# Optimization experiments

Measured on AMD Instinct MI355X. Metric: run time of the kernel, lower is better.

Reference implementation:

```python
import jax, jax.numpy as jnp
import numpy as np

B, T, X, H, Z, Y, G = 4096, 32, 256, 256, 128, 2, 128


def setup_inputs() -> dict:
    key = jax.random.key(0)
    ks = jax.random.split(key, 16)
    rn = lambda k, s, sc=0.05: jax.random.normal(k, s, dtype=jnp.float32) * sc
    n_days = jnp.concatenate([jnp.array([T], dtype=jnp.int32),
                              jax.random.randint(ks[2], (B - 1,), 1, T + 1).astype(jnp.int32)])
    return {
        "x": rn(ks[0], (B, T, X), 1.0),
        "y_true": jax.nn.softmax(jax.random.normal(ks[1], (B, T, Y), dtype=jnp.float32), axis=-1),
        "n_days": n_days,
        "z0": rn(ks[3], (B, Z), 1.0),
        "eps": rn(ks[4], (T, B, Z), 1.0),
        "W_ih": rn(ks[5], (3 * H, X)), "W_hh": rn(ks[6], (3 * H, H)),
        "b_ih": jnp.zeros((3 * H,), jnp.float32), "b_hh": jnp.zeros((3 * H,), jnp.float32),
        "Wph": rn(ks[7], (Z, X + H + Z)), "bph": jnp.zeros((Z,), jnp.float32),
        "Woh": rn(ks[8], (Z, X + H + Y + Z)), "boh": jnp.zeros((Z,), jnp.float32),
        "Wpm": rn(ks[9], (Z, Z)), "bpm": jnp.zeros((Z,), jnp.float32),
        "Wps": rn(ks[10], (Z, Z)), "bps": jnp.zeros((Z,), jnp.float32),
        "Wqm": rn(ks[11], (Z, Z)), "bqm": jnp.zeros((Z,), jnp.float32),
        "Wqs": rn(ks[12], (Z, Z)), "bqs": jnp.zeros((Z,), jnp.float32),
        "Wg": rn(ks[13], (G, H + Z)), "bg": jnp.zeros((G,), jnp.float32),
        "Wy": rn(ks[14], (Y, G)), "by": jnp.zeros((Y,), jnp.float32),
    }


def _forward(x, y_true, z0, eps, W_ih, W_hh, b_ih, b_hh, Wph, bph, Woh, boh,
             Wpm, bpm, Wps, bps, Wqm, bqm, Wqs, bqs, Wg, bg, Wy, by, n_days):
    xt = jnp.transpose(x, (1, 0, 2))       # [T, B, X]
    yt = jnp.transpose(y_true, (1, 0, 2))  # [T, B, Y]

    # --- GRU over time (torch nn.GRU gate math) ---
    def gru_step(h, xi):
        gi = xi @ W_ih.T + b_ih
        gh = h @ W_hh.T + b_hh
        ir, iz, inn = jnp.split(gi, 3, axis=-1)
        hr, hz, hn = jnp.split(gh, 3, axis=-1)
        r = jax.nn.sigmoid(ir + hr)
        u = jax.nn.sigmoid(iz + hz)
        n = jnp.tanh(inn + r * hn)
        h_new = (1.0 - u) * n + u * h
        return h_new, h_new

    h0 = jnp.zeros((x.shape[0], H), x.dtype)
    _, hs = jax.lax.scan(gru_step, h0, xt)  # [T, B, H]
    # pack/pad semantics: padded timesteps produce zero outputs
    valid = jnp.arange(T)[:, None] < n_days[None, :]  # [T, B]
    hs = jnp.where(valid[:, :, None], hs, 0.0)

    # --- sequential VAE latent scan: z_t depends on z_{t-1} ---
    def vmd_step(z, inputs):
        xi, hi, yi, ei = inputs
        hzp = jnp.tanh(jnp.concatenate([xi, hi, z], -1) @ Wph.T + bph)
        mp = hzp @ Wpm.T + bpm
        sp = jnp.sqrt(jnp.exp(hzp @ Wps.T + bps))
        hzq = jnp.tanh(jnp.concatenate([xi, hi, yi, z], -1) @ Woh.T + boh)
        mq = hzq @ Wqm.T + bqm
        sq = jnp.sqrt(jnp.exp(hzq @ Wqs.T + bqs))
        z_post = mq + sq * ei
        # kl_normal_normal(post || prior)
        kl = jnp.log(sp / sq) + (sq * sq + (mq - mp) ** 2) / (2.0 * sp * sp) - 0.5
        return z_post, (z_post, kl)

    _, (z_posts, kls_e) = jax.lax.scan(vmd_step, z0, (xt, hs, yt, eps))
    kls = jnp.sum(kls_e, axis=-1).T  # [B, T]

    hz = jnp.concatenate([jnp.transpose(hs, (1, 0, 2)),
                          jnp.transpose(z_posts, (1, 0, 2))], -1)  # [B, T, H+Z]
    g = jnp.tanh(hz @ Wg.T + bg)                     # [B, T, G]
    y_pred = jax.nn.softmax(g @ Wy.T + by, axis=-1)  # [B, T, Y]

    idx = n_days - 1
    b = jnp.arange(x.shape[0])
    g_T = g[b, idx]       # [B, G]
    y_T = y_pred[b, idx]  # [B, Y]
    return jnp.concatenate([g_T, y_T, kls], axis=-1)  # [B, G+Y+T]


def reference(x, y_true, n_days, z0, eps, W_ih, W_hh, b_ih, b_hh, Wph, bph,
              Woh, boh, Wpm, bpm, Wps, bps, Wqm, bqm, Wqs, bqs, Wg, bg, Wy, by):
    return _forward(x, y_true, z0, eps, W_ih, W_hh, b_ih, b_hh, Wph, bph, Woh,
                    boh, Wpm, bpm, Wps, bps, Wqm, bqm, Wqs, bqs, Wg, bg, Wy, by,
                    n_days)
```

## Files before the change

kernel.cpp:

```cpp
#include <hip/hip_runtime.h>

typedef unsigned short u16;
typedef short bf16x8 __attribute__((ext_vector_type(8)));
typedef float f32x4 __attribute__((ext_vector_type(4)));

__device__ __forceinline__ float bf2f(u16 v){
  union { unsigned u; float f; } x; x.u = ((unsigned)v) << 16; return x.f;
}
__device__ __forceinline__ u16 f2bf(float f){
  union { float f; unsigned u; } x; x.f = f;
  unsigned u = x.u;
  u += 0x7fffu + ((u >> 16) & 1u);
  return (u16)(u >> 16);
}
__device__ __forceinline__ unsigned pk_bf16(float lo, float hi){
  unsigned r;
  asm volatile("v_cvt_pk_bf16_f32 %0, %1, %2" : "=v"(r) : "v"(lo), "v"(hi));
  return r;
}
__device__ __forceinline__ float sigm(float x){ return 1.f/(1.f+__expf(-x)); }
__device__ __forceinline__ float tanh_s(float x){ return 1.f - 2.f/(__expf(2.f*x)+1.f); }
__device__ __forceinline__ f32x4 mfma16(bf16x8 a, bf16x8 b, f32x4 c){
  return __builtin_amdgcn_mfma_f32_16x16x32_bf16(a, b, c, 0, 0, 0);
}
__device__ __forceinline__ void gl2lds16(const void* g, void* l){
  __builtin_amdgcn_global_load_lds(
      (const __attribute__((address_space(1))) unsigned int*)g,
      (__attribute__((address_space(3))) unsigned int*)l, 16, 0, 0);
}

__global__ void prep_w(const float* __restrict__ W_ih, const float* __restrict__ W_hh,
                       const float* __restrict__ Wph, const float* __restrict__ Woh,
                       const float* __restrict__ Wpm, const float* __restrict__ Wps,
                       const float* __restrict__ Wqm, const float* __restrict__ Wqs,
                       const float* __restrict__ Wg,  const float* __restrict__ bph,
                       const float* __restrict__ boh,
                       u16* __restrict__ wsb, float* __restrict__ Woy, float* __restrict__ bpq)
{
  int idx = blockIdx.x*256 + threadIdx.x;
  if (idx < 196608){ wsb[idx] = f2bf(W_ih[idx]); return; }
  if (idx < 393216){ wsb[idx] = f2bf(W_hh[idx-196608]); return; }
  if (idx < 524288){ int j = idx-393216; int row = j>>9, col = j&511;
    float v = (row<128) ? Wph[row*640+col] : Woh[(row-128)*642+col];
    wsb[idx] = f2bf(v); return; }
  if (idx < 540672){ int j = idx-524288; int row=j>>7, col=j&127; wsb[idx]=f2bf(Wph[row*640+512+col]); return; }
  if (idx < 557056){ int j = idx-540672; int row=j>>7, col=j&127; wsb[idx]=f2bf(Woh[row*642+514+col]); return; }
  if (idx < 573440){ wsb[idx]=f2bf(Wpm[idx-557056]); return; }
  if (idx < 589824){ wsb[idx]=f2bf(Wps[idx-573440]); return; }
  if (idx < 606208){ wsb[idx]=f2bf(Wqm[idx-589824]); return; }
  if (idx < 622592){ wsb[idx]=f2bf(Wqs[idx-606208]); return; }
  if (idx < 671744){ wsb[idx]=f2bf(Wg[idx-622592]); return; }
  if (idx < 672000){ int j = idx-671744; int row=j>>1; Woy[j] = Woh[row*642+512+(j&1)]; return; }
  if (idx < 672256){ int j = idx-672000; bpq[j] = (j<128) ? bph[j] : boh[j-128]; return; }
}

__global__ void prep_b(const float* __restrict__ b_ih, const float* __restrict__ b_hh,
                       float* __restrict__ bsum)
{
  int j = threadIdx.x;
  if (j < 768) bsum[j] = b_ih[j] + (j < 512 ? b_hh[j] : 0.f);
}

__global__ void prep_x(const float* __restrict__ x, u16* __restrict__ xbf){
  int i = blockIdx.x*256 + threadIdx.x;
  if (i >= 4194304) return;
  const float4* src = (const float4*)(x + (size_t)i*8);
  float4 a = src[0], b = src[1];
  uint4 o;
  o.x = pk_bf16(a.x, a.y);
  o.y = pk_bf16(a.z, a.w);
  o.z = pk_bf16(b.x, b.y);
  o.w = pk_bf16(b.z, b.w);
  ((uint4*)xbf)[i] = o;
}

__global__ __launch_bounds__(512, 4) void gemm_bt(
  const u16* __restrict__ A1, const u16* __restrict__ A2, int K1, int Ktot,
  const u16* __restrict__ W, const float* __restrict__ bias,
  u16* __restrict__ C, int N, int mode,
  const float* __restrict__ yt, const float* __restrict__ Woy)
{
  const int m0 = blockIdx.x*128;
  const int n0 = blockIdx.y*256;
  const int tid = threadIdx.x;
  const int w = tid>>6, lane = tid&63, c = lane&15, g = lane>>4;
  const int wm = w>>2, wn = w&3;
  const int K2 = Ktot - K1;
  __shared__ __align__(16) u16 abuf[8*128*8];
  __shared__ __align__(16) u16 wbuf[8*256*8];
  f32x4 acc[4][4];
  #pragma unroll
  for (int i=0;i<4;++i)
    #pragma unroll
    for (int j=0;j<4;++j) acc[i][j] = (f32x4){0.f,0.f,0.f,0.f};
  const int nch = Ktot >> 6;
  for (int kc=0; kc<nch; ++kc){
    __syncthreads();
    #pragma unroll
    for (int i=0;i<2;++i){
      int ii = w*2 + i;
      int p = ii*64 + lane;
      int k8 = p>>7, row = p&127;
      int k = (kc<<6) + k8*8;
      const u16* src = (k < K1) ? (A1 + (size_t)(m0+row)*K1 + k)
                                : (A2 + (size_t)(m0+row)*K2 + (k-K1));
      gl2lds16(src, &abuf[ii*512]);
    }
    #pragma unroll
    for (int i=0;i<4;++i){
      int ii = w*4 + i;
      int p = ii*64 + lane;
      int k8 = p>>8, row = p&255;
      int k = (kc<<6) + k8*8;
      const u16* src = W + (size_t)(n0+row)*Ktot + k;
      gl2lds16(src, &wbuf[ii*512]);
    }
    __syncthreads();
    #pragma unroll
    for (int ks=0;ks<2;++ks){
      int k8 = ks*4 + g;
      bf16x8 a[4];
      #pragma unroll
      for (int mt=0;mt<4;++mt) a[mt] = *(const bf16x8*)&abuf[(k8*128 + wm*64 + mt*16 + c)*8];
      #pragma unroll
      for (int nt=0;nt<4;++nt){
        bf16x8 b = *(const bf16x8*)&wbuf[(k8*256 + wn*64 + nt*16 + c)*8];
        #pragma unroll
        for (int mt=0;mt<4;++mt)
          acc[mt][nt] = mfma16(a[mt], b, acc[mt][nt]);
      }
    }
  }
  #pragma unroll
  for (int nt=0;nt<4;++nt){
    int n = n0 + wn*64 + nt*16 + c;
    float bn = bias[n];
    float wy0 = 0.f, wy1 = 0.f;
    bool yfl = (mode==1) && (n >= 128);
    if (yfl){ wy0 = Woy[(n-128)*2]; wy1 = Woy[(n-128)*2+1]; }
    #pragma unroll
    for (int mt=0;mt<4;++mt){
      #pragma unroll
      for (int r=0;r<4;++r){
        size_t m = (size_t)m0 + wm*64 + mt*16 + g*4 + r;
        float v = acc[mt][nt][r] + bn;
        if (yfl) v += yt[2*m]*wy0 + yt[2*m+1]*wy1;
        C[m*(size_t)N + n] = f2bf(v);
      }
    }
  }
}

__global__ __launch_bounds__(1024) void gru_seq(
  const u16* __restrict__ GI, const u16* __restrict__ Whh,
  const float* __restrict__ bhh, const int* __restrict__ n_days,
  u16* __restrict__ hs)
{
  const int b0 = blockIdx.x*16;
  const int tid = threadIdx.x;
  const int w = tid>>6, lane = tid&63, c = lane&15, g = lane>>4;
  const int j0 = w*16 + g*4;
  __shared__ __align__(16) u16 hbuf[2][32*16*8];
  __shared__ __align__(16) u16 gibuf[3][16*768];
  __shared__ float bhnl[256];

  bf16x8 wa[3][8];
  #pragma unroll
  for (int gate=0; gate<3; ++gate)
    #pragma unroll
    for (int ks=0; ks<8; ++ks)
      wa[gate][ks] = *(const bf16x8*)&Whh[(size_t)(gate*256 + w*16 + c)*256 + ks*32 + g*8];

  if (tid < 256) bhnl[tid] = bhh[512 + tid];
  const int ndc = n_days[b0 + c];

  int so0, so1;
  { int pe = w*512 + lane*8; int row = pe/768, off = pe%768;
    so0 = (b0+row)*32*768 + (off ^ ((row&7)<<3)); }
  { int pe = (16+w)*512 + lane*8; int row = pe/768, off = pe%768;
    so1 = (b0+row)*32*768 + (off ^ ((row&7)<<3)); }
  const int rd0 = c*1536 + ((j0*2) ^ ((c&7)<<4));
  const int hroff = (g*16 + c)*16;
  const int hwoff = ((w*2 + (g>>1))*16 + c)*16 + (g&1)*8;
  u16* hsp = hs + ((size_t)(b0+c)*32)*256 + j0;

  float hprev[4] = {0.f,0.f,0.f,0.f};
  if (tid < 512) ((uint4*)hbuf[0])[tid] = make_uint4(0,0,0,0);

  gl2lds16(GI + so0,       (char*)gibuf[0] + w*1024);
  if (w < 8) gl2lds16(GI + so1, (char*)gibuf[0] + (16+w)*1024);
  gl2lds16(GI + so0 + 768, (char*)gibuf[1] + w*1024);
  if (w < 8) gl2lds16(GI + so1 + 768, (char*)gibuf[1] + (16+w)*1024);
  asm volatile("s_waitcnt vmcnt(0)" ::: "memory");
  __syncthreads();

  const u16* hr = hbuf[0];
  u16*       hw = hbuf[1];
  int cur = 0;
  #pragma unroll 1
  for (int t=0; t<32; ++t){
    if (t < 30){
      int nxt3 = cur >= 1 ? cur-1 : 2;
      const u16* gp = GI + (t+2)*768;
      gl2lds16(gp + so0, (char*)gibuf[nxt3] + w*1024);
      if (w < 8) gl2lds16(gp + so1, (char*)gibuf[nxt3] + (16+w)*1024);
    }
    if (t < 30){
      if (w < 8) asm volatile("s_waitcnt vmcnt(3)" ::: "memory");
      else       asm volatile("s_waitcnt vmcnt(2)" ::: "memory");
    } else if (t == 30){
      asm volatile("s_waitcnt vmcnt(1)" ::: "memory");
    }
    __builtin_amdgcn_sched_barrier(0);
    f32x4 aR = (f32x4){0.f,0.f,0.f,0.f};
    f32x4 aU = (f32x4){0.f,0.f,0.f,0.f};
    float4 bhn4 = *(const float4*)&bhnl[j0];
    f32x4 aN = (f32x4){bhn4.x, bhn4.y, bhn4.z, bhn4.w};
    #pragma unroll
    for (int ks=0; ks<8; ++ks){
      bf16x8 hf = *(const bf16x8*)((const char*)hr + hroff + ks*1024);
      aR = mfma16(wa[0][ks], hf, aR);
      aU = mfma16(wa[1][ks], hf, aU);
      aN = mfma16(wa[2][ks], hf, aN);
    }
    {
      const char* gib = (const char*)gibuf[cur];
      ushort4 gr_ = *(const ushort4*)(gib + rd0);
      ushort4 gu_ = *(const ushort4*)(gib + rd0 + 512);
      ushort4 gn_ = *(const ushort4*)(gib + rd0 + 1024);
      float h4[4];
      #pragma unroll
      for (int r=0; r<4; ++r){
        u16 grv = r==0?gr_.x : r==1?gr_.y : r==2?gr_.z : gr_.w;
        u16 guv = r==0?gu_.x : r==1?gu_.y : r==2?gu_.z : gu_.w;
        u16 gnv = r==0?gn_.x : r==1?gn_.y : r==2?gn_.z : gn_.w;
        float rr = sigm(bf2f(grv) + aR[r]);
        float uu = sigm(bf2f(guv) + aU[r]);
        float nn = tanh_s(bf2f(gnv) + rr*aN[r]);
        float h = nn + uu*(hprev[r]-nn);
        hprev[r] = h;
        h4[r] = h;
      }
      uint2 hpk;
      hpk.x = pk_bf16(h4[0], h4[1]);
      hpk.y = pk_bf16(h4[2], h4[3]);
      *(uint2*)((char*)hw + hwoff) = hpk;
      uint2 hst = (t < ndc) ? hpk : make_uint2(0u,0u);
      *(uint2*)(hsp + t*256) = hst;
    }
    asm volatile("s_waitcnt lgkmcnt(0)" ::: "memory");
    __builtin_amdgcn_sched_barrier(0);
    __builtin_amdgcn_s_barrier();
    __builtin_amdgcn_sched_barrier(0);
    { const u16* tmp = hr; hr = hw; hw = (u16*)tmp; }
    cur = cur==2 ? 0 : cur+1;
  }
}

__global__ __launch_bounds__(512) void vae_seq(
  const u16* __restrict__ HPQ, const float* __restrict__ z0,
  const float* __restrict__ eps, const int* __restrict__ n_days,
  const u16* __restrict__ Wm,
  const float* __restrict__ bpm, const float* __restrict__ bps,
  const float* __restrict__ bqm, const float* __restrict__ bqs,
  u16* __restrict__ zidx, float* __restrict__ out)
{
  const int b0 = blockIdx.x*16;
  const int tid = threadIdx.x, w = tid>>6, lane = tid&63, c = lane&15, g = lane>>4;
  const int j0 = w*16 + g*4;
  __shared__ __align__(16) u16 zbuf[16*16*8];
  __shared__ __align__(16) u16 hzpb[16*16*8];
  __shared__ __align__(16) u16 hzqb[16*16*8];
  __shared__ __align__(16) char hpql[3][8192];
  __shared__ __align__(16) char epsl[3][8192];
  __shared__ float klb[32][16][8];

  bf16x8 wf[6][4];
  #pragma unroll
  for (int mat=0;mat<6;++mat)
    #pragma unroll
    for (int ks=0;ks<4;++ks)
      wf[mat][ks] = *(const bf16x8*)&Wm[mat*16384 + (w*16+c)*128 + ks*32 + g*8];

  const float4 bpm4 = *(const float4*)(bpm + j0);
  const float4 bps4 = *(const float4*)(bps + j0);
  const float4 bqm4 = *(const float4*)(bqm + j0);
  const float4 bqs4 = *(const float4*)(bqs + j0);
  const int ndc = n_days[b0 + c];

  int soH, soE;
  { int p = (w*64 + lane)*16; int row = p/512, off = p%512;
    int so = off ^ ((row&7)<<4);
    soH = (b0+row)*32*256 + (so>>1);
    soE = (b0+row)*128 + (so>>2); }
  const int rdH = c*512 + ((j0*2) ^ ((c&7)<<4));
  const int rdE = c*512 + ((j0*4) ^ ((c&7)<<4));
  const int hroff = (g*16 + c)*16;
  const int hwoff = ((w*2 + (g>>1))*16 + c)*16 + (g&1)*8;

  if (tid < 256){
    int k8 = tid>>4, row = tid&15;
    const float* zp = z0 + (size_t)(b0+row)*128 + k8*8;
    uint4 o;
    o.x = pk_bf16(zp[0], zp[1]);
    o.y = pk_bf16(zp[2], zp[3]);
    o.z = pk_bf16(zp[4], zp[5]);
    o.w = pk_bf16(zp[6], zp[7]);
    ((uint4*)zbuf)[tid] = o;
  }
  gl2lds16(HPQ + soH,        hpql[0] + w*1024);
  gl2lds16(eps + soE,        epsl[0] + w*1024);
  gl2lds16(HPQ + soH + 256,  hpql[1] + w*1024);
  gl2lds16(eps + soE + 524288, epsl[1] + w*1024);
  asm volatile("s_waitcnt vmcnt(0)" ::: "memory");
  __syncthreads();

  uint2 zsel = make_uint2(0u,0u);
  int cur = 0;
  #pragma unroll 1
  for (int t=0; t<32; ++t){
    if (t < 30){
      int nxt3 = cur >= 1 ? cur-1 : 2;
      gl2lds16(HPQ + soH + (t+2)*256,           hpql[nxt3] + w*1024);
      gl2lds16(eps + soE + (size_t)(t+2)*524288, epsl[nxt3] + w*1024);
    }
    if (t < 30)      { asm volatile("s_waitcnt vmcnt(2)" ::: "memory"); }
    else if (t == 30){ asm volatile("s_waitcnt vmcnt(0)" ::: "memory"); }
    __builtin_amdgcn_sched_barrier(0);
    f32x4 accP = (f32x4){0,0,0,0}, accQ = (f32x4){0,0,0,0};
    #pragma unroll
    for (int ks=0;ks<4;++ks){
      bf16x8 zf = *(const bf16x8*)((const char*)zbuf + hroff + ks*1024);
      accP = mfma16(wf[0][ks], zf, accP);
      accQ = mfma16(wf[1][ks], zf, accQ);
    }
    {
      const char* hb_ = hpql[cur];
      ushort4 hp4 = *(const ushort4*)(hb_ + rdH);
      ushort4 hq4 = *(const ushort4*)(hb_ + rdH + 256);
      float p4[4], q4[4];
      #pragma unroll
      for (int r=0;r<4;++r){
        u16 pv = r==0?hp4.x : r==1?hp4.y : r==2?hp4.z : hp4.w;
        u16 qv = r==0?hq4.x : r==1?hq4.y : r==2?hq4.z : hq4.w;
        p4[r] = tanh_s(bf2f(pv) + accP[r]);
        q4[r] = tanh_s(bf2f(qv) + accQ[r]);
      }
      uint2 ppk, qpk;
      ppk.x = pk_bf16(p4[0], p4[1]);  ppk.y = pk_bf16(p4[2], p4[3]);
      qpk.x = pk_bf16(q4[0], q4[1]);  qpk.y = pk_bf16(q4[2], q4[3]);
      *(uint2*)((char*)hzpb + hwoff) = ppk;
      *(uint2*)((char*)hzqb + hwoff) = qpk;
    }
    asm volatile("s_waitcnt lgkmcnt(0)" ::: "memory");
    __builtin_amdgcn_sched_barrier(0);
    __builtin_amdgcn_s_barrier();
    __builtin_amdgcn_sched_barrier(0);
    {
      f32x4 aMP=(f32x4){0,0,0,0}, aAP=(f32x4){0,0,0,0};
      f32x4 aMQ=(f32x4){0,0,0,0}, aAQ=(f32x4){0,0,0,0};
      #pragma unroll
      for (int ks=0;ks<4;++ks){
        bf16x8 pf = *(const bf16x8*)((const char*)hzpb + hroff + ks*1024);
        bf16x8 qf = *(const bf16x8*)((const char*)hzqb + hroff + ks*1024);
        aMP = mfma16(wf[2][ks], pf, aMP);
        aAP = mfma16(wf[3][ks], pf, aAP);
        aMQ = mfma16(wf[4][ks], qf, aMQ);
        aAQ = mfma16(wf[5][ks], qf, aAQ);
      }
      float4 e4 = *(const float4*)(epsl[cur] + rdE);
      float kls = 0.f;
      float z4[4];
      #pragma unroll
      for (int r=0;r<4;++r){
        float mp = aMP[r]+(r==0?bpm4.x:r==1?bpm4.y:r==2?bpm4.z:bpm4.w);
        float ap = aAP[r]+(r==0?bps4.x:r==1?bps4.y:r==2?bps4.z:bps4.w);
        float mq = aMQ[r]+(r==0?bqm4.x:r==1?bqm4.y:r==2?bqm4.z:bqm4.w);
        float aq = aAQ[r]+(r==0?bqs4.x:r==1?bqs4.y:r==2?bqs4.z:bqs4.w);
        float ev = r==0?e4.x : r==1?e4.y : r==2?e4.z : e4.w;
        float z = mq + __expf(0.5f*aq)*ev;
        float d = mq - mp;
        kls += 0.5f*(ap-aq) + 0.5f*(__expf(aq)+d*d)*__expf(-ap) - 0.5f;
        z4[r] = z;
      }
      uint2 zpk;
      zpk.x = pk_bf16(z4[0], z4[1]);
      zpk.y = pk_bf16(z4[2], z4[3]);
      *(uint2*)((char*)zbuf + hwoff) = zpk;
      if (t == ndc-1) zsel = zpk;
      kls += __shfl_xor(kls, 16);
      kls += __shfl_xor(kls, 32);
      if (lane < 16) klb[t][c][w] = kls;
    }
    asm volatile("s_waitcnt lgkmcnt(0)" ::: "memory");
    __builtin_amdgcn_sched_barrier(0);
    __builtin_amdgcn_s_barrier();
    __builtin_amdgcn_sched_barrier(0);
    cur = cur==2 ? 0 : cur+1;
  }
  *(uint2*)(zidx + (size_t)(b0+c)*128 + j0) = zsel;
  {
    int t2 = tid>>4, c2 = tid&15;
    float s = 0.f;
    #pragma unroll
    for (int ww=0;ww<8;++ww) s += klb[t2][c2][ww];
    out[(size_t)(b0+c2)*162 + 130 + t2] = s;
  }
}

__global__ __launch_bounds__(128) void head_k(
  const u16* __restrict__ hs, const u16* __restrict__ zidx,
  const int* __restrict__ n_days, const u16* __restrict__ Wgb,
  const float* __restrict__ bg, const float* __restrict__ Wy,
  const float* __restrict__ by, float* __restrict__ out)
{
  const int b = blockIdx.x;
  const int tid = threadIdx.x;
  const int lane = tid & 63, wv = tid >> 6;
  __shared__ float hz[384];
  __shared__ float red[2][2];
  const int idx = n_days[b]-1;
  const u16* hrow = hs + ((size_t)b*32 + idx)*256;
  for (int k=tid; k<256; k+=128) hz[k] = bf2f(hrow[k]);
  hz[256+tid] = bf2f(zidx[(size_t)b*128 + tid]);
  __syncthreads();
  const u16* wrow = Wgb + (size_t)tid*384;
  float s = 0.f;
  #pragma unroll 4
  for (int k8=0;k8<48;++k8){
    bf16x8 wvv = *(const bf16x8*)&wrow[k8*8];
    #pragma unroll
    for (int e=0;e<8;++e) s += bf2f((u16)wvv[e]) * hz[k8*8+e];
  }
  float gv = tanh_s(s + bg[tid]);
  out[(size_t)b*162 + tid] = gv;
  float a0 = gv*Wy[tid], a1 = gv*Wy[128+tid];
  #pragma unroll
  for (int off=1; off<64; off<<=1){
    a0 += __shfl_xor(a0, off);
    a1 += __shfl_xor(a1, off);
  }
  if (lane == 0){ red[0][wv] = a0; red[1][wv] = a1; }
  __syncthreads();
  if (tid == 0){
    float l0 = by[0] + red[0][0] + red[0][1];
    float l1 = by[1] + red[1][0] + red[1][1];
    float mx = fmaxf(l0,l1);
    float e0 = __expf(l0-mx), e1 = __expf(l1-mx);
    float si = e0+e1;
    out[(size_t)b*162 + 128] = e0/si;
    out[(size_t)b*162 + 129] = e1/si;
  }
}

extern "C" void kernel_launch(void* const* d_in, const int* in_sizes, int n_in,
                              void* d_out, int out_size, void* d_ws, size_t ws_size,
                              hipStream_t stream)
{
  const float* x      = (const float*)d_in[0];
  const float* y_true = (const float*)d_in[1];
  const int*   n_days = (const int*)d_in[2];
  const float* z0     = (const float*)d_in[3];
  const float* eps    = (const float*)d_in[4];
  const float* W_ih   = (const float*)d_in[5];
  const float* W_hh   = (const float*)d_in[6];
  const float* b_ih   = (const float*)d_in[7];
  const float* b_hh   = (const float*)d_in[8];
  const float* Wph    = (const float*)d_in[9];
  const float* bph    = (const float*)d_in[10];
  const float* Woh    = (const float*)d_in[11];
  const float* boh    = (const float*)d_in[12];
  const float* Wpm    = (const float*)d_in[13];
  const float* bpm    = (const float*)d_in[14];
  const float* Wps    = (const float*)d_in[15];
  const float* bps    = (const float*)d_in[16];
  const float* Wqm    = (const float*)d_in[17];
  const float* bqm    = (const float*)d_in[18];
  const float* Wqs    = (const float*)d_in[19];
  const float* bqs    = (const float*)d_in[20];
  const float* Wg     = (const float*)d_in[21];
  const float* bg     = (const float*)d_in[22];
  const float* Wy     = (const float*)d_in[23];
  const float* by     = (const float*)d_in[24];
  (void)in_sizes; (void)n_in; (void)out_size; (void)ws_size;

  u16*   wsb = (u16*)d_ws;
  float* wsf = (float*)d_ws;
  u16* Wih_b = wsb + 0;
  u16* Whh_b = wsb + 196608;
  u16* Wc_b  = wsb + 393216;
  u16* Wz_b  = wsb + 524288;
  u16* Wg_b  = wsb + 622592;
  float* Woy  = wsf + 335872;
  float* bpq  = wsf + 336128;
  float* bsum = wsf + 336384;
  u16* xbf   = wsb + 674304;
  u16* GI    = wsb + 34228736;
  u16* hsB   = wsb + 134892032;
  u16* HPQ   = wsb + 168446464;
  u16* zidx  = wsb + 202000896;

  hipLaunchKernelGGL(prep_w, dim3(2626), dim3(256), 0, stream,
                     W_ih, W_hh, Wph, Woh, Wpm, Wps, Wqm, Wqs, Wg, bph, boh,
                     wsb, Woy, bpq);
  hipLaunchKernelGGL(prep_b, dim3(1), dim3(768), 0, stream, b_ih, b_hh, bsum);
  hipLaunchKernelGGL(prep_x, dim3(16384), dim3(256), 0, stream, x, xbf);
  hipLaunchKernelGGL(gemm_bt, dim3(1024,3), dim3(512), 0, stream,
                     xbf, xbf, 256, 256, Wih_b, bsum, GI, 768, 0,
                     (const float*)nullptr, (const float*)nullptr);
  hipLaunchKernelGGL(gru_seq, dim3(256), dim3(1024), 0, stream,
                     GI, Whh_b, b_hh, n_days, hsB);
  hipLaunchKernelGGL(gemm_bt, dim3(1024,1), dim3(512), 0, stream,
                     xbf, hsB, 256, 512, Wc_b, bpq, HPQ, 256, 1, y_true, Woy);
  hipLaunchKernelGGL(vae_seq, dim3(256), dim3(512), 0, stream,
                     HPQ, z0, eps, n_days, Wz_b, bpm, bps, bqm, bqs, zidx, (float*)d_out);
  hipLaunchKernelGGL(head_k, dim3(4096), dim3(128), 0, stream,
                     hsB, zidx, n_days, Wg_b, bg, Wy, by, (float*)d_out);
}
```

Measured before the change: 546.0 us.

## Sort batch by sequence length to skip padded GRU timesteps and GI rows

Adds a counting-sort kernel that orders batch rows by n_days descending. The input GEMM then computes GI only for valid (row,timestep) pairs in a time-major sorted layout, and the GRU loops only to the longest length in each 16-row group, writing zeros for the padded steps. Both GEMMs also stage their output tiles through LDS so global stores are coalesced, and the GRU raises wave priority around its MFMA block. The cost is an extra launch plus permutation indirection, and the per-group loop bound depends on how the input lengths are distributed.

```diff
diff --git a/kernel.cpp b/kernel.cpp
--- a/kernel.cpp
+++ b/kernel.cpp
@@ -74,47 +74,76 @@
   ((uint4*)xbf)[i] = o;
 }
 
-__global__ __launch_bounds__(512, 4) void gemm_bt(
-  const u16* __restrict__ A1, const u16* __restrict__ A2, int K1, int Ktot,
-  const u16* __restrict__ W, const float* __restrict__ bias,
-  u16* __restrict__ C, int N, int mode,
-  const float* __restrict__ yt, const float* __restrict__ Woy)
-{
-  const int m0 = blockIdx.x*128;
+__global__ void sort_days(const int* __restrict__ n_days, int* __restrict__ perm,
+                          int* __restrict__ nd_s, int* __restrict__ cnt)
+{
+  __shared__ int hist[34];
+  __shared__ int base[34];
+  __shared__ int cursor[34];
+  int tid = threadIdx.x;
+  if (tid < 34) hist[tid] = 0;
+  __syncthreads();
+  for (int i = tid; i < 4096; i += 1024) atomicAdd(&hist[n_days[i]], 1);
+  __syncthreads();
+  if (tid == 0){
+    int acc = 0;
+    for (int v = 32; v >= 1; --v){ base[v] = acc; acc += hist[v]; }
+    base[0] = acc;
+  }
+  __syncthreads();
+  if (tid < 33) cursor[tid] = base[tid];
+  if (tid < 32) cnt[tid] = base[tid];
+  __syncthreads();
+  for (int i = tid; i < 4096; i += 1024){
+    int v = n_days[i];
+    int pos = atomicAdd(&cursor[v], 1);
+    perm[pos] = i;
+    nd_s[pos] = v;
+  }
+}
+
+__global__ __launch_bounds__(512, 4) void gemm_gi(
+  const u16* __restrict__ A, const u16* __restrict__ W,
+  const float* __restrict__ bias, const int* __restrict__ perm,
+  const int* __restrict__ cnt, u16* __restrict__ C)
+{
+  const int t  = blockIdx.x >> 5;
+  const int rt = blockIdx.x & 31;
+  if (rt*128 >= cnt[t]) return;
   const int n0 = blockIdx.y*256;
   const int tid = threadIdx.x;
   const int w = tid>>6, lane = tid&63, c = lane&15, g = lane>>4;
   const int wm = w>>2, wn = w&3;
-  const int K2 = Ktot - K1;
-  __shared__ __align__(16) u16 abuf[8*128*8];
-  __shared__ __align__(16) u16 wbuf[8*256*8];
+  __shared__ __align__(16) char smem[49152];
+  u16* abuf = (u16*)smem;
+  u16* wbuf = (u16*)(smem + 16384);
+  u16* clds = (u16*)smem;
+
+  size_t asrc[2];
+  #pragma unroll
+  for (int i=0;i<2;++i){
+    int p = (w*2+i)*64 + lane;
+    int k8 = p>>7, row = p&127;
+    asrc[i] = ((size_t)perm[rt*128 + row]*32 + t)*256 + k8*8;
+  }
+  size_t wsrc[4];
+  #pragma unroll
+  for (int i=0;i<4;++i){
+    int p = (w*4+i)*64 + lane;
+    int k8 = p>>8, row = p&255;
+    wsrc[i] = (size_t)(n0+row)*256 + k8*8;
+  }
   f32x4 acc[4][4];
   #pragma unroll
   for (int i=0;i<4;++i)
     #pragma unroll
     for (int j=0;j<4;++j) acc[i][j] = (f32x4){0.f,0.f,0.f,0.f};
-  const int nch = Ktot >> 6;
-  for (int kc=0; kc<nch; ++kc){
-    __syncthreads();
-    #pragma unroll
-    for (int i=0;i<2;++i){
-      int ii = w*2 + i;
-      int p = ii*64 + lane;
-      int k8 = p>>7, row = p&127;
-      int k = (kc<<6) + k8*8;
-      const u16* src = (k < K1) ? (A1 + (size_t)(m0+row)*K1 + k)
-                                : (A2 + (size_t)(m0+row)*K2 + (k-K1));
-      gl2lds16(src, &abuf[ii*512]);
-    }
-    #pragma unroll
-    for (int i=0;i<4;++i){
-      int ii = w*4 + i;
-      int p = ii*64 + lane;
-      int k8 = p>>8, row = p&255;
-      int k = (kc<<6) + k8*8;
-      const u16* src = W + (size_t)(n0+row)*Ktot + k;
-      gl2lds16(src, &wbuf[ii*512]);
-    }
+  for (int kc=0; kc<4; ++kc){
+    __syncthreads();
+    #pragma unroll
+    for (int i=0;i<2;++i) gl2lds16(A + asrc[i] + kc*64, &abuf[(w*2+i)*512]);
+    #pragma unroll
+    for (int i=0;i<4;++i) gl2lds16(W + wsrc[i] + kc*64, &wbuf[(w*4+i)*512]);
     __syncthreads();
     #pragma unroll
     for (int ks=0;ks<2;++ks){
@@ -131,37 +160,143 @@
       }
     }
   }
-  #pragma unroll
-  for (int nt=0;nt<4;++nt){
-    int n = n0 + wn*64 + nt*16 + c;
-    float bn = bias[n];
-    float wy0 = 0.f, wy1 = 0.f;
-    bool yfl = (mode==1) && (n >= 128);
-    if (yfl){ wy0 = Woy[(n-128)*2]; wy1 = Woy[(n-128)*2+1]; }
-    #pragma unroll
-    for (int mt=0;mt<4;++mt){
-      #pragma unroll
-      for (int r=0;r<4;++r){
-        size_t m = (size_t)m0 + wm*64 + mt*16 + g*4 + r;
-        float v = acc[mt][nt][r] + bn;
-        if (yfl) v += yt[2*m]*wy0 + yt[2*m+1]*wy1;
-        C[m*(size_t)N + n] = f2bf(v);
-      }
-    }
-  }
-}
-
-__global__ __launch_bounds__(1024) void gru_seq(
+  __syncthreads();
+  const size_t crow = (size_t)t*4096 + rt*128;
+  #pragma unroll
+  for (int nh=0; nh<2; ++nh){
+    if ((wn>>1) == nh){
+      #pragma unroll
+      for (int nt=0;nt<4;++nt){
+        int n = n0 + wn*64 + nt*16 + c;
+        float bn = bias[n];
+        int lc = (wn&1)*64 + nt*16 + c;
+        #pragma unroll
+        for (int mt=0;mt<4;++mt){
+          int lr = wm*64 + mt*16 + g*4;
+          #pragma unroll
+          for (int r=0;r<4;++r)
+            clds[(lr+r)*136 + lc] = f2bf(acc[mt][nt][r] + bn);
+        }
+      }
+    }
+    __syncthreads();
+    #pragma unroll
+    for (int p=0;p<4;++p){
+      int idx = p*512 + tid;
+      int row = idx>>4, ch = idx&15;
+      *(uint4*)(C + (crow+row)*768 + n0 + nh*128 + ch*8)
+        = *(const uint4*)&clds[row*136 + ch*8];
+    }
+    __syncthreads();
+  }
+}
+
+__global__ __launch_bounds__(512, 4) void gemm_hpq(
+  const u16* __restrict__ A1, const u16* __restrict__ A2,
+  const u16* __restrict__ W, const float* __restrict__ bias,
+  const float* __restrict__ yt, const float* __restrict__ Woy,
+  u16* __restrict__ C)
+{
+  const int m0 = blockIdx.x*128;
+  const int tid = threadIdx.x;
+  const int w = tid>>6, lane = tid&63, c = lane&15, g = lane>>4;
+  const int wm = w>>2, wn = w&3;
+  __shared__ __align__(16) char smem[49152];
+  u16* abuf = (u16*)smem;
+  u16* wbuf = (u16*)(smem + 16384);
+  u16* clds = (u16*)smem;
+
+  size_t asrc[2];
+  #pragma unroll
+  for (int i=0;i<2;++i){
+    int p = (w*2+i)*64 + lane;
+    int k8 = p>>7, row = p&127;
+    asrc[i] = (size_t)(m0+row)*256 + k8*8;
+  }
+  size_t wsrc[4];
+  #pragma unroll
+  for (int i=0;i<4;++i){
+    int p = (w*4+i)*64 + lane;
+    int k8 = p>>8, row = p&255;
+    wsrc[i] = (size_t)row*512 + k8*8;
+  }
+  f32x4 acc[4][4];
+  #pragma unroll
+  for (int i=0;i<4;++i)
+    #pragma unroll
+    for (int j=0;j<4;++j) acc[i][j] = (f32x4){0.f,0.f,0.f,0.f};
+  for (int kc=0; kc<8; ++kc){
+    __syncthreads();
+    const u16* Ab = (kc < 4) ? A1 : A2;
+    int ko = (kc & 3)*64;
+    #pragma unroll
+    for (int i=0;i<2;++i) gl2lds16(Ab + asrc[i] + ko, &abuf[(w*2+i)*512]);
+    #pragma unroll
+    for (int i=0;i<4;++i) gl2lds16(W + wsrc[i] + kc*64, &wbuf[(w*4+i)*512]);
+    __syncthreads();
+    #pragma unroll
+    for (int ks=0;ks<2;++ks){
+      int k8 = ks*4 + g;
+      bf16x8 a[4];
+      #pragma unroll
+      for (int mt=0;mt<4;++mt) a[mt] = *(const bf16x8*)&abuf[(k8*128 + wm*64 + mt*16 + c)*8];
+      #pragma unroll
+      for (int nt=0;nt<4;++nt){
+        bf16x8 b = *(const bf16x8*)&wbuf[(k8*256 + wn*64 + nt*16 + c)*8];
+        #pragma unroll
+        for (int mt=0;mt<4;++mt)
+          acc[mt][nt] = mfma16(a[mt], b, acc[mt][nt]);
+      }
+    }
+  }
+  __syncthreads();
+  #pragma unroll
+  for (int nh=0; nh<2; ++nh){
+    if ((wn>>1) == nh){
+      #pragma unroll
+      for (int nt=0;nt<4;++nt){
+        int n = wn*64 + nt*16 + c;
+        float bn = bias[n];
+        float wy0 = 0.f, wy1 = 0.f;
+        bool yfl = (n >= 128);
+        if (yfl){ wy0 = Woy[(n-128)*2]; wy1 = Woy[(n-128)*2+1]; }
+        int lc = (wn&1)*64 + nt*16 + c;
+        #pragma unroll
+        for (int mt=0;mt<4;++mt){
+          int lr = wm*64 + mt*16 + g*4;
+          #pragma unroll
+          for (int r=0;r<4;++r){
+            size_t m = (size_t)m0 + lr + r;
+            float v = acc[mt][nt][r] + bn;
+            if (yfl) v += yt[2*m]*wy0 + yt[2*m+1]*wy1;
+            clds[(lr+r)*136 + lc] = f2bf(v);
+          }
+        }
+      }
+    }
+    __syncthreads();
+    #pragma unroll
+    for (int p=0;p<4;++p){
+      int idx = p*512 + tid;
+      int row = idx>>4, ch = idx&15;
+      *(uint4*)(C + (size_t)(m0+row)*256 + nh*128 + ch*8)
+        = *(const uint4*)&clds[row*136 + ch*8];
+    }
+    __syncthreads();
+  }
+}
+
+__global__ __launch_bounds__(1024, 4) void gru_seq(
   const u16* __restrict__ GI, const u16* __restrict__ Whh,
-  const float* __restrict__ bhh, const int* __restrict__ n_days,
-  u16* __restrict__ hs)
+  const float* __restrict__ bhh, const int* __restrict__ perm,
+  const int* __restrict__ nd_s, u16* __restrict__ hs)
 {
   const int b0 = blockIdx.x*16;
   const int tid = threadIdx.x;
   const int w = tid>>6, lane = tid&63, c = lane&15, g = lane>>4;
   const int j0 = w*16 + g*4;
-  __shared__ __align__(16) u16 hbuf[2][32*16*8];
-  __shared__ __align__(16) u16 gibuf[3][16*768];
+  __shared__ __align__(16) u16 hbuf[2][4096];
+  __shared__ __align__(16) u16 gibuf[3][12288];
   __shared__ float bhnl[256];
 
   bf16x8 wa[3][8];
@@ -172,25 +307,29 @@
       wa[gate][ks] = *(const bf16x8*)&Whh[(size_t)(gate*256 + w*16 + c)*256 + ks*32 + g*8];
 
   if (tid < 256) bhnl[tid] = bhh[512 + tid];
-  const int ndc = n_days[b0 + c];
+  const int ndc   = nd_s[b0 + c];
+  const int bound = nd_s[b0];
+  const int ob    = perm[b0 + c];
 
   int so0, so1;
-  { int pe = w*512 + lane*8; int row = pe/768, off = pe%768;
-    so0 = (b0+row)*32*768 + (off ^ ((row&7)<<3)); }
-  { int pe = (16+w)*512 + lane*8; int row = pe/768, off = pe%768;
-    so1 = (b0+row)*32*768 + (off ^ ((row&7)<<3)); }
+  { int pe = w*512 + lane*8; int row = pe/768, off = pe - row*768;
+    so0 = (b0+row)*768 + (off ^ ((row&7)<<3)); }
+  { int pe = (16+w)*512 + lane*8; int row = pe/768, off = pe - row*768;
+    so1 = (b0+row)*768 + (off ^ ((row&7)<<3)); }
   const int rd0 = c*1536 + ((j0*2) ^ ((c&7)<<4));
   const int hroff = (g*16 + c)*16;
   const int hwoff = ((w*2 + (g>>1))*16 + c)*16 + (g&1)*8;
-  u16* hsp = hs + ((size_t)(b0+c)*32)*256 + j0;
+  u16* hsp = hs + (size_t)ob*8192 + j0;
 
   float hprev[4] = {0.f,0.f,0.f,0.f};
   if (tid < 512) ((uint4*)hbuf[0])[tid] = make_uint4(0,0,0,0);
 
-  gl2lds16(GI + so0,       (char*)gibuf[0] + w*1024);
+  const size_t PL = 3145728;
+  int p1 = (bound > 1) ? 1 : 0;
+  gl2lds16(GI + so0, (char*)gibuf[0] + w*1024);
   if (w < 8) gl2lds16(GI + so1, (char*)gibuf[0] + (16+w)*1024);
-  gl2lds16(GI + so0 + 768, (char*)gibuf[1] + w*1024);
-  if (w < 8) gl2lds16(GI + so1 + 768, (char*)gibuf[1] + (16+w)*1024);
+  gl2lds16(GI + (size_t)p1*PL + so0, (char*)gibuf[1] + w*1024);
+  if (w < 8) gl2lds16(GI + (size_t)p1*PL + so1, (char*)gibuf[1] + (16+w)*1024);
   asm volatile("s_waitcnt vmcnt(0)" ::: "memory");
   __syncthreads();
 
@@ -198,24 +337,25 @@
   u16*       hw = hbuf[1];
   int cur = 0;
   #pragma unroll 1
-  for (int t=0; t<32; ++t){
-    if (t < 30){
+  for (int t=0; t<bound; ++t){
+    {
+      int pf = (t+2 < bound) ? t+2 : bound-1;
       int nxt3 = cur >= 1 ? cur-1 : 2;
-      const u16* gp = GI + (t+2)*768;
-      gl2lds16(gp + so0, (char*)gibuf[nxt3] + w*1024);
-      if (w < 8) gl2lds16(gp + so1, (char*)gibuf[nxt3] + (16+w)*1024);
-    }
-    if (t < 30){
-      if (w < 8) asm volatile("s_waitcnt vmcnt(3)" ::: "memory");
-      else       asm volatile("s_waitcnt vmcnt(2)" ::: "memory");
-    } else if (t == 30){
-      asm volatile("s_waitcnt vmcnt(1)" ::: "memory");
-    }
+      gl2lds16(GI + (size_t)pf*PL + so0, (char*)gibuf[nxt3] + w*1024);
+      if (w < 8) gl2lds16(GI + (size_t)pf*PL + so1, (char*)gibuf[nxt3] + (16+w)*1024);
+    }
+    const char* gib = (const char*)gibuf[cur];
+    ushort4 gr_ = *(const ushort4*)(gib + rd0);
+    ushort4 gu_ = *(const ushort4*)(gib + rd0 + 512);
+    ushort4 gn_ = *(const ushort4*)(gib + rd0 + 1024);
+    if (w < 8) asm volatile("s_waitcnt vmcnt(3)" ::: "memory");
+    else       asm volatile("s_waitcnt vmcnt(2)" ::: "memory");
     __builtin_amdgcn_sched_barrier(0);
     f32x4 aR = (f32x4){0.f,0.f,0.f,0.f};
     f32x4 aU = (f32x4){0.f,0.f,0.f,0.f};
     float4 bhn4 = *(const float4*)&bhnl[j0];
     f32x4 aN = (f32x4){bhn4.x, bhn4.y, bhn4.z, bhn4.w};
+    __builtin_amdgcn_s_setprio(1);
     #pragma unroll
     for (int ks=0; ks<8; ++ks){
       bf16x8 hf = *(const bf16x8*)((const char*)hr + hroff + ks*1024);
@@ -223,11 +363,8 @@
       aU = mfma16(wa[1][ks], hf, aU);
       aN = mfma16(wa[2][ks], hf, aN);
     }
+    __builtin_amdgcn_s_setprio(0);
     {
-      const char* gib = (const char*)gibuf[cur];
-      ushort4 gr_ = *(const ushort4*)(gib + rd0);
-      ushort4 gu_ = *(const ushort4*)(gib + rd0 + 512);
-      ushort4 gn_ = *(const ushort4*)(gib + rd0 + 1024);
       float h4[4];
       #pragma unroll
       for (int r=0; r<4; ++r){
@@ -255,6 +392,8 @@
     { const u16* tmp = hr; hr = hw; hw = (u16*)tmp; }
     cur = cur==2 ? 0 : cur+1;
   }
+  for (int t=bound; t<32; ++t)
+    *(uint2*)(hsp + t*256) = make_uint2(0u,0u);
 }
 
 __global__ __launch_bounds__(512) void vae_seq(
@@ -308,9 +447,9 @@
     o.w = pk_bf16(zp[6], zp[7]);
     ((uint4*)zbuf)[tid] = o;
   }
-  gl2lds16(HPQ + soH,        hpql[0] + w*1024);
-  gl2lds16(eps + soE,        epsl[0] + w*1024);
-  gl2lds16(HPQ + soH + 256,  hpql[1] + w*1024);
+  gl2lds16(HPQ + soH,          hpql[0] + w*1024);
+  gl2lds16(eps + soE,          epsl[0] + w*1024);
+  gl2lds16(HPQ + soH + 256,    hpql[1] + w*1024);
   gl2lds16(eps + soE + 524288, epsl[1] + w*1024);
   asm volatile("s_waitcnt vmcnt(0)" ::: "memory");
   __syncthreads();
@@ -321,7 +460,7 @@
   for (int t=0; t<32; ++t){
     if (t < 30){
       int nxt3 = cur >= 1 ? cur-1 : 2;
-      gl2lds16(HPQ + soH + (t+2)*256,           hpql[nxt3] + w*1024);
+      gl2lds16(HPQ + soH + (t+2)*256,            hpql[nxt3] + w*1024);
       gl2lds16(eps + soE + (size_t)(t+2)*524288, epsl[nxt3] + w*1024);
     }
     if (t < 30)      { asm volatile("s_waitcnt vmcnt(2)" ::: "memory"); }
@@ -486,6 +625,7 @@
 
   u16*   wsb = (u16*)d_ws;
   float* wsf = (float*)d_ws;
+  int*   wsi = (int*)d_ws;
   u16* Wih_b = wsb + 0;
   u16* Whh_b = wsb + 196608;
   u16* Wc_b  = wsb + 393216;
@@ -494,24 +634,28 @@
   float* Woy  = wsf + 335872;
   float* bpq  = wsf + 336128;
   float* bsum = wsf + 336384;
-  u16* xbf   = wsb + 674304;
-  u16* GI    = wsb + 34228736;
-  u16* hsB   = wsb + 134892032;
-  u16* HPQ   = wsb + 168446464;
-  u16* zidx  = wsb + 202000896;
+  int* perm   = wsi + 337152;
+  int* nd_s   = wsi + 341248;
+  int* cnt    = wsi + 345344;
+  u16* xbf   = wsb + 690752;
+  u16* GI    = wsb + 34245184;
+  u16* hsB   = wsb + 134908480;
+  u16* HPQ   = wsb + 168462912;
+  u16* zidx  = wsb + 202017344;
 
   hipLaunchKernelGGL(prep_w, dim3(2626), dim3(256), 0, stream,
                      W_ih, W_hh, Wph, Woh, Wpm, Wps, Wqm, Wqs, Wg, bph, boh,
                      wsb, Woy, bpq);
   hipLaunchKernelGGL(prep_b, dim3(1), dim3(768), 0, stream, b_ih, b_hh, bsum);
   hipLaunchKernelGGL(prep_x, dim3(16384), dim3(256), 0, stream, x, xbf);
-  hipLaunchKernelGGL(gemm_bt, dim3(1024,3), dim3(512), 0, stream,
-                     xbf, xbf, 256, 256, Wih_b, bsum, GI, 768, 0,
-                     (const float*)nullptr, (const float*)nullptr);
+  hipLaunchKernelGGL(sort_days, dim3(1), dim3(1024), 0, stream,
+                     n_days, perm, nd_s, cnt);
+  hipLaunchKernelGGL(gemm_gi, dim3(1024,3), dim3(512), 0, stream,
+                     xbf, Wih_b, bsum, perm, cnt, GI);
   hipLaunchKernelGGL(gru_seq, dim3(256), dim3(1024), 0, stream,
-                     GI, Whh_b, b_hh, n_days, hsB);
-  hipLaunchKernelGGL(gemm_bt, dim3(1024,1), dim3(512), 0, stream,
-                     xbf, hsB, 256, 512, Wc_b, bpq, HPQ, 256, 1, y_true, Woy);
+                     GI, Whh_b, b_hh, perm, nd_s, hsB);
+  hipLaunchKernelGGL(gemm_hpq, dim3(1024), dim3(512), 0, stream,
+                     xbf, hsB, Wc_b, bpq, y_true, Woy, HPQ);
   hipLaunchKernelGGL(vae_seq, dim3(256), dim3(512), 0, stream,
                      HPQ, z0, eps, n_days, Wz_b, bpm, bps, bqm, bqs, zidx, (float*)d_out);
   hipLaunchKernelGGL(head_k, dim3(4096), dim3(128), 0, stream,
```

Result: faster. 510.3 us (-6.6%).
